# Optimization experiments

Hardware: AMD Instinct MI355X
Metric: run time of the kernel (lower is better)

The kernel has to match this reference:

```python
import jax, jax.numpy as jnp
import numpy as np

N, D, C, P = 256, 1024, 4, 46  # nodes, embedding_dim, max children, num dependency labels
NEG = -1e30  # masked-out candidate value for the max-reduce


def setup_inputs() -> dict:
    key = jax.random.key(0)
    k1, k2 = jax.random.split(key)
    embeddings = jax.random.normal(k1, (N, D), dtype=jnp.float32)
    # Xavier-uniform init of the per-dependency [D,D] matrices, as in _init_params
    scale = float(np.sqrt(6.0 / (D + D)))
    params = jax.random.uniform(k2, (P, D, D), dtype=jnp.float32, minval=-scale, maxval=scale)
    # Build a random tree in topological order: children of node i have index < i;
    # node N-1 is the root. Padded child slots are masked out.
    rng = np.random.default_rng(0)
    c_idx = np.zeros((N, C), dtype=np.int32)
    c_mask = np.zeros((N, C), dtype=bool)
    for i in range(1, N):
        n_children = int(rng.integers(0, C + 1))  # 0 => leaf-like internal node
        c_idx[i] = rng.integers(0, i, size=C)
        c_mask[i, :n_children] = True
    c_mask[N - 1, :] = True  # root always has children
    c_dep = rng.integers(0, P, size=(N, C)).astype(np.int32)
    return {
        "embeddings": embeddings,
        "params": params,
        "children_idx": jnp.asarray(c_idx),
        "children_dep": jnp.asarray(c_dep),
        "children_mask": jnp.asarray(c_mask),
    }


def reference(embeddings, params, children_idx, children_dep, children_mask):
    """Tree-structured dependency encoder.

    For each node i (children first, topological order):
      leaf:     z_i = x_i
      internal: cand_c = params[dep_c] * relu(z_child_c)[None, :]   # [D, D] per child
                mult   = max over children of cand_c                 # [D, D]
                z_i    = x_i @ mult                                  # [D]
    Returns the root embedding, shape [1, D] (matches torch output).
    """
    n_nodes, d = embeddings.shape

    def step(z, inp):
        i, c_idx, c_dep, c_mask = inp
        child_z = jax.nn.relu(z[c_idx])                      # [C, D]
        cand = params[c_dep] * child_z[:, None, :]           # [C, D, D]
        cand = jnp.where(c_mask[:, None, None], cand, NEG)
        mult = jnp.max(cand, axis=0)                         # [D, D]
        x = embeddings[i]                                    # [D]
        z_i = jnp.where(jnp.any(c_mask), x @ mult, x)
        return z.at[i].set(z_i), None

    z0 = jnp.zeros_like(embeddings)
    idxs = jnp.arange(n_nodes)
    z, _ = jax.lax.scan(step, z0, (idxs, children_idx, children_dep, children_mask))
    return z[-1:]  # root node is last in topological order -> [1, D]
```

## Files before the change

kernel.cpp:

```cpp
#include <hip/hip_runtime.h>
#include <hip/hip_fp16.h>
#include <cstddef>

#define NN 256
#define DD 1024
#define CC 4
#define NP 46
#define NT 512
#define ROOT (NN - 1)

typedef unsigned int uint4v __attribute__((ext_vector_type(4)));

__device__ __half g_Pth[NP][DD][DD];

__global__ __launch_bounds__(256) void transpose_kernel(
    const float* __restrict__ par) {
  __shared__ float tile[64][65];
  const int b = blockIdx.x;
  const int p = b >> 8;
  const int t = b & 255;
  const int tr = (t >> 4) << 6;
  const int tc = (t & 15) << 6;
  const int tid = threadIdx.x;
  const float* src = par + ((size_t)p << 20);
  __half* dst = &g_Pth[p][0][0];

#pragma unroll
  for (int k = 0; k < 4; ++k) {
    const int idx = tid + (k << 8);
    const int row = idx >> 4;
    const int c4 = (idx & 15) << 2;
    const float4 v = *(const float4*)(src + (size_t)(tr + row) * DD + tc + c4);
    float* tp = &tile[row][c4];
    tp[0] = v.x; tp[1] = v.y; tp[2] = v.z; tp[3] = v.w;
  }
  __syncthreads();

#pragma unroll
  for (int s = 0; s < 2; ++s) {
    const int u = tid + (s << 8);
    const int c = u >> 3;
    const int r8 = (u & 7) << 3;
    unsigned int h[4];
#pragma unroll
    for (int i = 0; i < 4; ++i) {
      const __half2 hh =
          __floats2half2_rn(tile[r8 + 2 * i][c], tile[r8 + 2 * i + 1][c]);
      h[i] = *(const unsigned int*)&hh;
    }
    uint4v uu = {h[0], h[1], h[2], h[3]};
    __builtin_nontemporal_store(
        uu, (uint4v*)(dst + (size_t)(tc + c) * DD + tr + r8));
  }
}

struct St {
  float2 p0, p1, p2, p3;
  float x0, x1;
};

__device__ __forceinline__ float4 relu4(float4 v) {
  float4 r;
  r.x = fmaxf(v.x, 0.f); r.y = fmaxf(v.y, 0.f);
  r.z = fmaxf(v.z, 0.f); r.w = fmaxf(v.w, 0.f);
  return r;
}

__device__ __forceinline__ void ld_stage(St& S, int e,
                                         const __half* __restrict__ pt,
                                         const float* __restrict__ emb,
                                         const short* e_meta, const short* e_node,
                                         int j0, int r2) {
  const int meta = e_meta[e];
  const int dep = meta & 0x1FFF;
  const __half* hb = pt + (((size_t)dep) << 20) + (((size_t)j0) << 10) + r2;
  S.p0 = __half22float2(*(const __half2*)(hb));
  S.p1 = __half22float2(*(const __half2*)(hb + DD));
  S.p2 = __half22float2(*(const __half2*)(hb + 2 * DD));
  S.p3 = __half22float2(*(const __half2*)(hb + 3 * DD));
  if (meta & 0x8000) {
    const float2 xx = *(const float2*)(emb + (((size_t)e_node[e]) << 10) + r2);
    S.x0 = xx.x; S.x1 = xx.y;
  }
}

__device__ __forceinline__ float2 mul2s(float2 a, float s) {
  float2 r; r.x = a.x * s; r.y = a.y * s; return r;
}
__device__ __forceinline__ float2 max2(float2 a, float2 b) {
  float2 r; r.x = fmaxf(a.x, b.x); r.y = fmaxf(a.y, b.y); return r;
}

__device__ __forceinline__ void cmp_stage(const St& S, int e, float2& m0, float2& m1,
                                          float2& m2, float2& m3,
                                          float (*z_loc)[4], float (*s_part)[4],
                                          const short* e_child, const short* e_meta,
                                          const short* e_node, int tid) {
  const int meta = e_meta[e];
  const float4 u = relu4(*(const float4*)z_loc[e_child[e]]);
  if (meta & (1 << 14)) {
    m0 = mul2s(S.p0, u.x); m1 = mul2s(S.p1, u.y);
    m2 = mul2s(S.p2, u.z); m3 = mul2s(S.p3, u.w);
  } else {
    m0 = max2(m0, mul2s(S.p0, u.x)); m1 = max2(m1, mul2s(S.p1, u.y));
    m2 = max2(m2, mul2s(S.p2, u.z)); m3 = max2(m3, mul2s(S.p3, u.w));
  }
  if (meta & 0x8000) {
    float4 acc;
    acc.x = fmaf(S.x1, m0.y, S.x0 * m0.x);
    acc.y = fmaf(S.x1, m1.y, S.x0 * m1.x);
    acc.z = fmaf(S.x1, m2.y, S.x0 * m2.x);
    acc.w = fmaf(S.x1, m3.y, S.x0 * m3.x);
#pragma unroll
    for (int off = 1; off < 64; off <<= 1) {
      acc.x += __shfl_xor(acc.x, off, 64);
      acc.y += __shfl_xor(acc.y, off, 64);
      acc.z += __shfl_xor(acc.z, off, 64);
      acc.w += __shfl_xor(acc.w, off, 64);
    }
    if ((tid & 63) == 0) *(float4*)s_part[tid >> 6] = acc;
    __syncthreads();
    if (tid < 4) {
      float s = 0.f;
#pragma unroll
      for (int k = 0; k < 8; ++k) s += s_part[k][tid];
      z_loc[e_node[e]][tid] = s;
    }
    __syncthreads();
  }
}

__global__ __launch_bounds__(NT, 1) void walk_kernel(
    const float* __restrict__ emb, const int* __restrict__ cidx,
    const int* __restrict__ cdep, const unsigned char* __restrict__ cmask,
    float* __restrict__ out) {
  __shared__ float z_loc[NN][4];
  __shared__ short s_ci[NN][CC];
  __shared__ short s_cd[NN][CC];
  __shared__ short s_nc[NN];
  __shared__ int s_pfx[NN];
  __shared__ unsigned char s_reach[NN];
  __shared__ short s_e_child[NN * CC];
  __shared__ short s_e_meta[NN * CC];
  __shared__ short s_e_node[NN * CC];
  __shared__ int s_NE;
  __shared__ int s_flag;
  __shared__ float s_part[8][4];

  const int tid = threadIdx.x;
  const int j0 = blockIdx.x << 2;
  const int r2 = tid << 1;
  const __half* pt = &g_Pth[0][0][0];

  if (tid == 0)
    s_flag = (cmask[1021] == 1 && cmask[1022] == 1 && cmask[1023] == 1);
  __syncthreads();
  const bool m_u8 = (s_flag != 0);
  const int* m32 = (const int*)cmask;
  if (tid < NN) {
    int nc = 0;
#pragma unroll
    for (int c = 0; c < CC; ++c) {
      bool mk = m_u8 ? (cmask[tid * CC + c] != 0) : (m32[tid * CC + c] != 0);
      if (mk) {
        s_ci[tid][nc] = (short)cidx[tid * CC + c];
        s_cd[tid][nc] = (short)cdep[tid * CC + c];
        ++nc;
      }
    }
    s_nc[tid] = (short)nc;
    s_reach[tid] = (tid == ROOT) ? 1 : 0;
  }
  __syncthreads();

  for (int it = 0; it < NN + 2; ++it) {
    if (tid == 0) s_flag = 0;
    __syncthreads();
    if (tid < NN && s_reach[tid] && s_nc[tid] > 0) {
      for (int c = 0; c < s_nc[tid]; ++c) {
        const int ch = s_ci[tid][c];
        if (!s_reach[ch]) { s_reach[ch] = 1; s_flag = 1; }
      }
    }
    __syncthreads();
    const int chg = s_flag;
    __syncthreads();
    if (!chg) break;
  }

  const int wgt = (tid < NN && s_reach[tid] && s_nc[tid] > 0) ? (int)s_nc[tid] : 0;
  if (tid < NN) s_pfx[tid] = wgt;
  __syncthreads();
  for (int off = 1; off < NN; off <<= 1) {
    int v = 0;
    if (tid < NN && tid >= off) v = s_pfx[tid - off];
    __syncthreads();
    if (tid < NN) s_pfx[tid] += v;
    __syncthreads();
  }
  if (tid < NN && wgt > 0) {
    const int st = s_pfx[tid] - wgt;
    for (int c = 0; c < wgt; ++c) {
      s_e_child[st + c] = s_ci[tid][c];
      int meta = (int)s_cd[tid][c];
      if (c == 0) meta |= 1 << 14;
      if (c == wgt - 1) meta |= 1 << 15;
      s_e_meta[st + c] = (short)meta;
      s_e_node[st + c] = (short)tid;
    }
  }
  if (tid == NN - 1) s_NE = s_pfx[NN - 1];

  if (tid < NN) {
    const float4 e = *(const float4*)(emb + (((size_t)tid) << 10) + j0);
    *(float4*)z_loc[tid] = e;
  }
  __syncthreads();
  const int NE = s_NE;

  St A, B, C, D;
  float2 m0, m1, m2, m3;
  if (NE > 0) ld_stage(A, 0, pt, emb, s_e_meta, s_e_node, j0, r2);
  if (NE > 1) ld_stage(B, 1, pt, emb, s_e_meta, s_e_node, j0, r2);
  if (NE > 2) ld_stage(C, 2, pt, emb, s_e_meta, s_e_node, j0, r2);
  int e = 0;
  while (e < NE) {
    if (e + 3 < NE) ld_stage(D, e + 3, pt, emb, s_e_meta, s_e_node, j0, r2);
    cmp_stage(A, e, m0, m1, m2, m3, z_loc, s_part, s_e_child, s_e_meta, s_e_node, tid);
    if (++e >= NE) break;
    if (e + 3 < NE) ld_stage(A, e + 3, pt, emb, s_e_meta, s_e_node, j0, r2);
    cmp_stage(B, e, m0, m1, m2, m3, z_loc, s_part, s_e_child, s_e_meta, s_e_node, tid);
    if (++e >= NE) break;
    if (e + 3 < NE) ld_stage(B, e + 3, pt, emb, s_e_meta, s_e_node, j0, r2);
    cmp_stage(C, e, m0, m1, m2, m3, z_loc, s_part, s_e_child, s_e_meta, s_e_node, tid);
    if (++e >= NE) break;
    if (e + 3 < NE) ld_stage(C, e + 3, pt, emb, s_e_meta, s_e_node, j0, r2);
    cmp_stage(D, e, m0, m1, m2, m3, z_loc, s_part, s_e_child, s_e_meta, s_e_node, tid);
    ++e;
  }

  if (tid < 4) out[j0 + tid] = z_loc[ROOT][tid];
}

extern "C" void kernel_launch(void* const* d_in, const int* in_sizes, int n_in,
                              void* d_out, int out_size, void* d_ws, size_t ws_size,
                              hipStream_t stream) {
  const float* emb = (const float*)d_in[0];
  const float* par = (const float*)d_in[1];
  const int* cidx = (const int*)d_in[2];
  const int* cdep = (const int*)d_in[3];
  const unsigned char* cmask = (const unsigned char*)d_in[4];
  float* out = (float*)d_out;

  hipLaunchKernelGGL(transpose_kernel, dim3(NP * 256), dim3(256), 0, stream, par);
  hipLaunchKernelGGL(walk_kernel, dim3(256), dim3(NT), 0, stream, emb, cidx,
                     cdep, cmask, out);
}
```

Measured before the change: 130.4 us.

## Make transpose blocks loop over column tiles with register-prefetched loads

The transpose kernel now launches 16 blocks per parameter matrix instead of 256. Each block handles a 64-row strip and loops over the 16 column tiles, prefetching the next tile's global loads into registers while it converts and stores the current tile. This is meant to hide load latency and cut per-block launch overhead. In exchange the grid shrinks to 736 blocks and each tile iteration adds a second barrier, which may lower memory-level parallelism across the GPU.

Result: slower. 138.6 us (+6.3%).

```diff
diff --git a/kernel.cpp b/kernel.cpp
--- a/kernel.cpp
+++ b/kernel.cpp
@@ -17,40 +17,60 @@
     const float* __restrict__ par) {
   __shared__ float tile[64][65];
   const int b = blockIdx.x;
-  const int p = b >> 8;
-  const int t = b & 255;
-  const int tr = (t >> 4) << 6;
-  const int tc = (t & 15) << 6;
+  const int p = b >> 4;
+  const int rb = b & 15;
   const int tid = threadIdx.x;
-  const float* src = par + ((size_t)p << 20);
+  const float* src = par + ((size_t)p << 20) + ((size_t)(rb << 6) << 10);
   __half* dst = &g_Pth[p][0][0];
 
+  float4 v[4];
 #pragma unroll
   for (int k = 0; k < 4; ++k) {
     const int idx = tid + (k << 8);
     const int row = idx >> 4;
     const int c4 = (idx & 15) << 2;
-    const float4 v = *(const float4*)(src + (size_t)(tr + row) * DD + tc + c4);
-    float* tp = &tile[row][c4];
-    tp[0] = v.x; tp[1] = v.y; tp[2] = v.z; tp[3] = v.w;
-  }
-  __syncthreads();
-
-#pragma unroll
-  for (int s = 0; s < 2; ++s) {
-    const int u = tid + (s << 8);
-    const int c = u >> 3;
-    const int r8 = (u & 7) << 3;
-    unsigned int h[4];
-#pragma unroll
-    for (int i = 0; i < 4; ++i) {
-      const __half2 hh =
-          __floats2half2_rn(tile[r8 + 2 * i][c], tile[r8 + 2 * i + 1][c]);
-      h[i] = *(const unsigned int*)&hh;
-    }
-    uint4v uu = {h[0], h[1], h[2], h[3]};
-    __builtin_nontemporal_store(
-        uu, (uint4v*)(dst + (size_t)(tc + c) * DD + tr + r8));
+    v[k] = *(const float4*)(src + (size_t)row * DD + c4);
+  }
+
+  for (int cb = 0; cb < 16; ++cb) {
+#pragma unroll
+    for (int k = 0; k < 4; ++k) {
+      const int idx = tid + (k << 8);
+      const int row = idx >> 4;
+      const int c4 = (idx & 15) << 2;
+      float* tp = &tile[row][c4];
+      tp[0] = v[k].x; tp[1] = v[k].y; tp[2] = v[k].z; tp[3] = v[k].w;
+    }
+    __syncthreads();
+
+    if (cb + 1 < 16) {
+      const float* s2 = src + ((cb + 1) << 6);
+#pragma unroll
+      for (int k = 0; k < 4; ++k) {
+        const int idx = tid + (k << 8);
+        const int row = idx >> 4;
+        const int c4 = (idx & 15) << 2;
+        v[k] = *(const float4*)(s2 + (size_t)row * DD + c4);
+      }
+    }
+
+#pragma unroll
+    for (int s = 0; s < 2; ++s) {
+      const int u = tid + (s << 8);
+      const int c = u >> 3;
+      const int r8 = (u & 7) << 3;
+      unsigned int h[4];
+#pragma unroll
+      for (int i = 0; i < 4; ++i) {
+        const __half2 hh =
+            __floats2half2_rn(tile[r8 + 2 * i][c], tile[r8 + 2 * i + 1][c]);
+        h[i] = *(const unsigned int*)&hh;
+      }
+      uint4v uu = {h[0], h[1], h[2], h[3]};
+      __builtin_nontemporal_store(
+          uu, (uint4v*)(dst + (size_t)((cb << 6) + c) * DD + (rb << 6) + r8));
+    }
+    __syncthreads();
   }
 }
 
@@ -252,7 +272,7 @@
   const unsigned char* cmask = (const unsigned char*)d_in[4];
   float* out = (float*)d_out;
 
-  hipLaunchKernelGGL(transpose_kernel, dim3(NP * 256), dim3(256), 0, stream, par);
+  hipLaunchKernelGGL(transpose_kernel, dim3(NP * 16), dim3(256), 0, stream, par);
   hipLaunchKernelGGL(walk_kernel, dim3(256), dim3(NT), 0, stream, emb, cidx,
                      cdep, cmask, out);
 }
```
